# Performance work log

Hardware: AMD Instinct MI355X
Metric: run time of the kernel (lower is better)

## Reference

```python
import jax, jax.numpy as jnp
import numpy as np

NEG_SLOPE = 0.2
EPS = 1e-16


def gat_conv(x, edge_index, W, att_src, att_dst, bias, heads, out_ch, concat):
    """PyG-style GATConv (eval mode, add_self_loops=True)."""
    N = x.shape[0]
    h = (x @ W).reshape(N, heads, out_ch)              # [N,H,C]
    loop = jnp.arange(N, dtype=edge_index.dtype)
    src = jnp.concatenate([edge_index[0], loop])       # [E+N]
    dst = jnp.concatenate([edge_index[1], loop])
    a_src = jnp.sum(h * att_src, axis=-1)              # [N,H]
    a_dst = jnp.sum(h * att_dst, axis=-1)
    e = jax.nn.leaky_relu(a_src[src] + a_dst[dst], NEG_SLOPE)  # [E+N,H]
    # segment softmax over destination nodes
    m = jax.ops.segment_max(e, dst, num_segments=N)
    e = jnp.exp(e - m[dst])
    s = jax.ops.segment_sum(e, dst, num_segments=N)
    alpha = e / (s[dst] + EPS)                         # [E+N,H]
    msg = h[src] * alpha[..., None]                    # [E+N,H,C]
    out = jax.ops.segment_sum(msg, dst, num_segments=N)  # [N,H,C]
    out = out.reshape(N, heads * out_ch) if concat else out.mean(axis=1)
    return out + bias


def setup_inputs() -> dict:
    key = jax.random.key(0)
    ks = jax.random.split(key, 11)
    N, F, E = 100000, 128, 1600000
    H1, C1 = 4, 16
    H2, C2 = 1, 16
    return {
        "x": jax.random.normal(ks[0], (N, F), dtype=jnp.float32),
        "edge_index": jax.random.randint(ks[1], (2, E), 0, N, dtype=jnp.int64) if jax.config.jax_enable_x64 else jax.random.randint(ks[1], (2, E), 0, N).astype(jnp.int32),
        "W1": jax.random.normal(ks[2], (F, H1 * C1), dtype=jnp.float32) * 0.1,
        "att_src1": jax.random.normal(ks[3], (H1, C1), dtype=jnp.float32) * 0.1,
        "att_dst1": jax.random.normal(ks[4], (H1, C1), dtype=jnp.float32) * 0.1,
        "bias1": jax.random.normal(ks[5], (H1 * C1,), dtype=jnp.float32) * 0.1,
        "W2": jax.random.normal(ks[6], (H1 * C1, H2 * C2), dtype=jnp.float32) * 0.1,
        "att_src2": jax.random.normal(ks[7], (H2, C2), dtype=jnp.float32) * 0.1,
        "att_dst2": jax.random.normal(ks[8], (H2, C2), dtype=jnp.float32) * 0.1,
        "bias2": jax.random.normal(ks[9], (C2,), dtype=jnp.float32) * 0.1,
    }


def reference(x, edge_index, W1, att_src1, att_dst1, bias1, W2, att_src2, att_dst2, bias2):
    # dropout is identity in eval mode
    h = gat_conv(x, edge_index, W1, att_src1, att_dst1, bias1, heads=4, out_ch=16, concat=True)
    h = jax.nn.elu(h)
    h = gat_conv(h, edge_index, W2, att_src2, att_dst2, bias2, heads=1, out_ch=16, concat=False)
    return jax.nn.log_softmax(h, axis=1)
```

## Files before the change

kernel.cpp:

```cpp
#include <hip/hip_runtime.h>
#include <hip/hip_fp16.h>
#include <hip/hip_bf16.h>
#include <math.h>


#define LRELU(v) ((v) > 0.f ? (v) : 0.2f * (v))
#define BSH 8
#define BCAP 5120
#define CHK 8192

typedef __attribute__((ext_vector_type(8))) short short8;
typedef __attribute__((ext_vector_type(8))) _Float16 half8;
typedef __attribute__((ext_vector_type(4))) _Float16 half4;
typedef __attribute__((ext_vector_type(4))) float float4v;

static __device__ __forceinline__ short f2bf(float f) {
    __hip_bfloat16 b = __float2bfloat16(f);
    return *reinterpret_cast<short*>(&b);
}

__global__ __launch_bounds__(256) void k_pre(const int* __restrict__ ei, int* __restrict__ cursor,
                                             int* __restrict__ stage, int E, int NBK,
                                             const float* __restrict__ x,
                                             const float* __restrict__ W1,
                                             const float* __restrict__ att_src1,
                                             const float* __restrict__ att_dst1,
                                             __half* __restrict__ h1,
                                             float* __restrict__ a_src, float* __restrict__ a_dst,
                                             int N, int GS) {
    __shared__ __align__(16) char smem[80 * 136 * 2];
    int tid = threadIdx.x;
    if (blockIdx.x < GS) {
        int* hist = (int*)smem;
        int* cnt2 = hist + 512;
        int* base = cnt2 + 512;
        int e0 = blockIdx.x * CHK;
        int nedge = E - e0; if (nedge > CHK) nedge = CHK;
        for (int i = tid; i < 512; i += 256) { hist[i] = 0; cnt2[i] = 0; }
        __syncthreads();
        for (int j = tid; j < nedge; j += 256) {
            int d = ei[E + e0 + j];
            atomicAdd(&hist[d >> BSH], 1);
        }
        __syncthreads();
        for (int b = tid; b < NBK; b += 256) {
            int c = hist[b];
            if (c > 0) base[b] = b * BCAP + atomicAdd(&cursor[b], c);
        }
        __syncthreads();
        for (int j = tid; j < nedge; j += 256) {
            int s = ei[e0 + j];
            int d = ei[E + e0 + j];
            int b = d >> BSH;
            int r = atomicAdd(&cnt2[b], 1);
            stage[base[b] + r] = s | ((d & ((1 << BSH) - 1)) << 17);
        }
    } else {
        short* wt = (short*)smem;
        for (int i = tid; i < 128 * 64; i += 256) {
            int k = i >> 6, c = i & 63;
            wt[c * 136 + k] = f2bf(W1[i]);
        }
        for (int i = tid; i < 16 * 128; i += 256) {
            int col = i >> 7, k = i & 127;
            float v = 0.f;
            if (col < 8) {
                int h = col & 3;
                const float* att = (col < 4) ? att_src1 : att_dst1;
                #pragma unroll
                for (int c = 0; c < 16; c++) v += W1[k * 64 + h * 16 + c] * att[h * 16 + c];
            }
            wt[(64 + col) * 136 + k] = f2bf(v);
        }
        __syncthreads();
        int wave = tid >> 6, lane = tid & 63;
        int m = lane & 15, q = lane >> 4;
        int nbase = (blockIdx.x - GS) * 64 + wave * 16;
        int anode = nbase + m;
        bool rowok = anode < N;
        const float* xrow = x + (size_t)(rowok ? anode : 0) * 128 + q * 8;

        float4v acc[5];
        #pragma unroll
        for (int ct = 0; ct < 5; ct++)
            #pragma unroll
            for (int r = 0; r < 4; r++) acc[ct][r] = 0.f;

        #pragma unroll
        for (int kc = 0; kc < 4; kc++) {
            float4 u0 = make_float4(0.f, 0.f, 0.f, 0.f), u1 = u0;
            if (rowok) {
                u0 = *(const float4*)(xrow + kc * 32);
                u1 = *(const float4*)(xrow + kc * 32 + 4);
            }
            short8 af;
            af[0] = f2bf(u0.x); af[1] = f2bf(u0.y); af[2] = f2bf(u0.z); af[3] = f2bf(u0.w);
            af[4] = f2bf(u1.x); af[5] = f2bf(u1.y); af[6] = f2bf(u1.z); af[7] = f2bf(u1.w);
            #pragma unroll
            for (int ct = 0; ct < 5; ct++) {
                short8 bf = *(const short8*)&wt[(ct * 16 + m) * 136 + kc * 32 + q * 8];
                acc[ct] = __builtin_amdgcn_mfma_f32_16x16x32_bf16(af, bf, acc[ct], 0, 0, 0);
            }
        }
        #pragma unroll
        for (int ct = 0; ct < 4; ct++) {
            #pragma unroll
            for (int r = 0; r < 4; r++) {
                int n = nbase + q * 4 + r;
                if (n < N) h1[(size_t)n * 64 + ct * 16 + m] = __float2half(acc[ct][r]);
            }
        }
        #pragma unroll
        for (int r = 0; r < 4; r++) {
            int n = nbase + q * 4 + r;
            if (n < N) {
                float v = acc[4][r];
                if (m < 4) a_src[n * 4 + m] = v;
                else if (m < 8) a_dst[n * 4 + (m - 4)] = v;
            }
        }
    }
}

__global__ __launch_bounds__(256) void k_build(const int* __restrict__ stage,
                                               const int* __restrict__ cursor,
                                               int* __restrict__ row_start,
                                               int* __restrict__ csr,
                                               int NBK, int E, int N) {
    __shared__ int cnt[256];
    __shared__ int lb[256];
    __shared__ int cur[256];
    __shared__ int sA[256];
    int b = blockIdx.x, tid = threadIdx.x;
    int nodes0 = b << BSH;
    int nnodes = N - nodes0; if (nnodes > 256) nnodes = 256;
    int partial = 0;
    for (int i = tid; i < b; i += 256) partial += cursor[i];
    sA[tid] = partial;
    __syncthreads();
    for (int off = 128; off >= 1; off >>= 1) {
        if (tid < off) sA[tid] += sA[tid + off];
        __syncthreads();
    }
    int ebase = sA[0];
    int ecnt = cursor[b];
    __syncthreads();
    if (b == 0 && tid == 0) row_start[N] = E + N;
    const int* sbk = stage + b * BCAP;
    cnt[tid] = (tid < nnodes) ? 1 : 0;
    __syncthreads();
    for (int e = tid; e < ecnt; e += 256) {
        int l = (sbk[e] >> 17) & 255;
        atomicAdd(&cnt[l], 1);
    }
    __syncthreads();
    int myc = cnt[tid];
    sA[tid] = myc;
    __syncthreads();
    for (int off = 1; off < 256; off <<= 1) {
        int r = sA[tid] + ((tid >= off) ? sA[tid - off] : 0);
        __syncthreads();
        sA[tid] = r;
        __syncthreads();
    }
    int gb = ebase + nodes0;
    lb[tid] = sA[tid] - myc;
    cur[tid] = 1;
    __syncthreads();
    if (tid < nnodes) {
        row_start[nodes0 + tid] = gb + lb[tid];
        csr[gb + lb[tid]] = nodes0 + tid;
    }
    __syncthreads();
    for (int e = tid; e < ecnt; e += 256) {
        int v = sbk[e];
        int l = (v >> 17) & 255;
        int src = v & 0x1FFFF;
        int r = atomicAdd(&cur[l], 1);
        csr[gb + lb[l] + r] = src;
    }
}

__global__ __launch_bounds__(256) void k_agg1f(const int* __restrict__ row_start,
                                               const int* __restrict__ csr_src,
                                               const float* __restrict__ a_src,
                                               const float* __restrict__ a_dst,
                                               const __half* __restrict__ h1,
                                               const float* __restrict__ bias,
                                               const float* __restrict__ W2,
                                               const float* __restrict__ att_src2,
                                               const float* __restrict__ att_dst2,
                                               __half* __restrict__ h2,
                                               float* __restrict__ a_src2,
                                               float* __restrict__ a_dst2, int N) {
    __shared__ float sW2[64 * 16];
    __shared__ float sAs[16], sAd[16];
    int tid = threadIdx.x;
    for (int i = tid; i < 1024; i += 256) sW2[i] = W2[i];
    if (tid < 16) { sAs[tid] = att_src2[tid]; sAd[tid] = att_dst2[tid]; }
    __syncthreads();
    int wave = tid >> 6, lane = tid & 63;
    int grp = lane >> 3, sub = lane & 3, par = (lane >> 2) & 1;
    int node = blockIdx.x * 32 + wave * 8 + grp;
    if (node >= N) return;
    int row = row_start[node];
    int deg = row_start[node + 1] - row;
    float adm = a_dst[node * 4 + sub];
    const _Float16* hb = (const _Float16*)h1 + sub * 16;
    const int* cp = csr_src + row + par;
    float A[16];
    #pragma unroll
    for (int c = 0; c < 16; c++) A[c] = 0.f;
    float sh = 0.f;
    int c0 = 0, c1 = 0, c2 = 0, c3 = 0;
    if (deg >= 8) { c0 = cp[0]; c1 = cp[2]; c2 = cp[4]; c3 = cp[6]; }
    int j = 0;
    for (; j + 8 <= deg; j += 8) {
        int s0 = c0, s1 = c1, s2 = c2, s3 = c3;
        float x0 = a_src[s0 * 4 + sub] + adm;
        float x1 = a_src[s1 * 4 + sub] + adm;
        float x2 = a_src[s2 * 4 + sub] + adm;
        float x3 = a_src[s3 * 4 + sub] + adm;
        half8 p0 = *(const half8*)(hb + (size_t)s0 * 64);
        half8 q0 = *(const half8*)(hb + (size_t)s0 * 64 + 8);
        half8 p1 = *(const half8*)(hb + (size_t)s1 * 64);
        half8 q1 = *(const half8*)(hb + (size_t)s1 * 64 + 8);
        half8 p2 = *(const half8*)(hb + (size_t)s2 * 64);
        half8 q2 = *(const half8*)(hb + (size_t)s2 * 64 + 8);
        half8 p3 = *(const half8*)(hb + (size_t)s3 * 64);
        half8 q3 = *(const half8*)(hb + (size_t)s3 * 64 + 8);
        if (j + 16 <= deg) {
            c0 = cp[j + 8]; c1 = cp[j + 10]; c2 = cp[j + 12]; c3 = cp[j + 14];
        }
        float e0 = __expf(fmaxf(x0, 0.2f * x0));
        float e1 = __expf(fmaxf(x1, 0.2f * x1));
        float e2 = __expf(fmaxf(x2, 0.2f * x2));
        float e3 = __expf(fmaxf(x3, 0.2f * x3));
        sh += (e0 + e1) + (e2 + e3);
        #pragma unroll
        for (int c = 0; c < 8; c++) {
            A[c]     += e0 * (float)p0[c] + e1 * (float)p1[c]
                      + e2 * (float)p2[c] + e3 * (float)p3[c];
            A[c + 8] += e0 * (float)q0[c] + e1 * (float)q1[c]
                      + e2 * (float)q2[c] + e3 * (float)q3[c];
        }
    }
    for (; j < deg; j += 2) {
        int idx = j + par;
        if (idx < deg) {
            int s = csr_src[row + idx];
            float xv = a_src[s * 4 + sub] + adm;
            half8 p = *(const half8*)(hb + (size_t)s * 64);
            half8 q = *(const half8*)(hb + (size_t)s * 64 + 8);
            float e = __expf(fmaxf(xv, 0.2f * xv));
            sh += e;
            #pragma unroll
            for (int c = 0; c < 8; c++) {
                A[c]     += e * (float)p[c];
                A[c + 8] += e * (float)q[c];
            }
        }
    }
    sh += __shfl_xor(sh, 4, 64);
    #pragma unroll
    for (int c = 0; c < 16; c++) A[c] += __shfl_xor(A[c], 4, 64);
    float iv = 1.f / (sh + 1e-16f);
    const float4* bb = (const float4*)bias + sub * 4;
    float o[16];
    #pragma unroll
    for (int c4 = 0; c4 < 4; c4++) {
        float4 b = bb[c4];
        float o0 = A[c4 * 4 + 0] * iv + b.x;
        float o1 = A[c4 * 4 + 1] * iv + b.y;
        float o2 = A[c4 * 4 + 2] * iv + b.z;
        float o3 = A[c4 * 4 + 3] * iv + b.w;
        o[c4 * 4 + 0] = (o0 > 0.f) ? o0 : (__expf(o0) - 1.f);
        o[c4 * 4 + 1] = (o1 > 0.f) ? o1 : (__expf(o1) - 1.f);
        o[c4 * 4 + 2] = (o2 > 0.f) ? o2 : (__expf(o2) - 1.f);
        o[c4 * 4 + 3] = (o3 > 0.f) ? o3 : (__expf(o3) - 1.f);
    }
    float pk[8];
    #pragma unroll
    for (int kk = 0; kk < 8; kk++) pk[kk] = 0.f;
    #pragma unroll
    for (int cc = 0; cc < 16; cc++) {
        float ov = o[cc];
        const float* wr = &sW2[(sub * 16 + cc) * 16 + par * 8];
        #pragma unroll
        for (int kk = 0; kk < 8; kk++) pk[kk] += ov * wr[kk];
    }
    #pragma unroll
    for (int kk = 0; kk < 8; kk++) {
        pk[kk] += __shfl_xor(pk[kk], 1, 64);
        pk[kk] += __shfl_xor(pk[kk], 2, 64);
    }
    if (sub == 0) {
        union { __half2 hh[4]; float4 f; } u;
        u.hh[0] = __floats2half2_rn(pk[0], pk[1]);
        u.hh[1] = __floats2half2_rn(pk[2], pk[3]);
        u.hh[2] = __floats2half2_rn(pk[4], pk[5]);
        u.hh[3] = __floats2half2_rn(pk[6], pk[7]);
        *(float4*)&h2[(size_t)node * 16 + par * 8] = u.f;
    }
    float ps = 0.f, pd = 0.f;
    #pragma unroll
    for (int kk = 0; kk < 8; kk++) {
        ps += pk[kk] * sAs[par * 8 + kk];
        pd += pk[kk] * sAd[par * 8 + kk];
    }
    ps += __shfl_xor(ps, 4, 64);
    pd += __shfl_xor(pd, 4, 64);
    if (sub == 0 && par == 0) { a_src2[node] = ps; a_dst2[node] = pd; }
}

__global__ __launch_bounds__(256) void k_agg2(const int* __restrict__ row_start,
                                              const int* __restrict__ csr_src,
                                              const float* __restrict__ a_src,
                                              const float* __restrict__ a_dst,
                                              const __half* __restrict__ h2,
                                              const float* __restrict__ bias,
                                              float* __restrict__ out, int N) {
    int tid = threadIdx.x;
    int wave = tid >> 6, lane = tid & 63;
    int grp = lane >> 4, sub = lane & 3, par = (lane >> 2) & 3;
    int node = blockIdx.x * 16 + wave * 4 + grp;
    if (node >= N) return;
    int row = row_start[node];
    int deg = row_start[node + 1] - row;
    float ad = a_dst[node];
    const _Float16* hb = (const _Float16*)h2 + sub * 4;
    const int* cp = csr_src + row + par;
    float A0 = 0.f, A1 = 0.f, A2 = 0.f, A3 = 0.f;
    float sh = 0.f;
    int c0 = 0, c1 = 0, c2 = 0, c3 = 0;
    if (deg >= 16) { c0 = cp[0]; c1 = cp[4]; c2 = cp[8]; c3 = cp[12]; }
    int j = 0;
    for (; j + 16 <= deg; j += 16) {
        int s0 = c0, s1 = c1, s2 = c2, s3 = c3;
        float x0 = a_src[s0] + ad;
        float x1 = a_src[s1] + ad;
        float x2 = a_src[s2] + ad;
        float x3 = a_src[s3] + ad;
        half4 v0 = *(const half4*)(hb + (size_t)s0 * 16);
        half4 v1 = *(const half4*)(hb + (size_t)s1 * 16);
        half4 v2 = *(const half4*)(hb + (size_t)s2 * 16);
        half4 v3 = *(const half4*)(hb + (size_t)s3 * 16);
        if (j + 32 <= deg) {
            c0 = cp[j + 16]; c1 = cp[j + 20]; c2 = cp[j + 24]; c3 = cp[j + 28];
        }
        float e0 = __expf(fmaxf(x0, 0.2f * x0));
        float e1 = __expf(fmaxf(x1, 0.2f * x1));
        float e2 = __expf(fmaxf(x2, 0.2f * x2));
        float e3 = __expf(fmaxf(x3, 0.2f * x3));
        sh += (e0 + e1) + (e2 + e3);
        A0 += e0 * (float)v0[0] + e1 * (float)v1[0] + e2 * (float)v2[0] + e3 * (float)v3[0];
        A1 += e0 * (float)v0[1] + e1 * (float)v1[1] + e2 * (float)v2[1] + e3 * (float)v3[1];
        A2 += e0 * (float)v0[2] + e1 * (float)v1[2] + e2 * (float)v2[2] + e3 * (float)v3[2];
        A3 += e0 * (float)v0[3] + e1 * (float)v1[3] + e2 * (float)v2[3] + e3 * (float)v3[3];
    }
    for (; j < deg; j += 4) {
        int idx = j + par;
        if (idx < deg) {
            int s = csr_src[row + idx];
            float xv = a_src[s] + ad;
            half4 v = *(const half4*)(hb + (size_t)s * 16);
            float e = __expf(fmaxf(xv, 0.2f * xv));
            sh += e;
            A0 += e * (float)v[0];
            A1 += e * (float)v[1];
            A2 += e * (float)v[2];
            A3 += e * (float)v[3];
        }
    }
    sh += __shfl_xor(sh, 4, 64);  sh += __shfl_xor(sh, 8, 64);
    A0 += __shfl_xor(A0, 4, 64);  A0 += __shfl_xor(A0, 8, 64);
    A1 += __shfl_xor(A1, 4, 64);  A1 += __shfl_xor(A1, 8, 64);
    A2 += __shfl_xor(A2, 4, 64);  A2 += __shfl_xor(A2, 8, 64);
    A3 += __shfl_xor(A3, 4, 64);  A3 += __shfl_xor(A3, 8, 64);
    float iv = 1.f / (sh + 1e-16f);
    float4 b = ((const float4*)bias)[sub];
    float v0 = A0 * iv + b.x;
    float v1 = A1 * iv + b.y;
    float v2 = A2 * iv + b.z;
    float v3 = A3 * iv + b.w;
    float mx = fmaxf(fmaxf(v0, v1), fmaxf(v2, v3));
    mx = fmaxf(mx, __shfl_xor(mx, 1, 64));
    mx = fmaxf(mx, __shfl_xor(mx, 2, 64));
    float se = __expf(v0 - mx) + __expf(v1 - mx) + __expf(v2 - mx) + __expf(v3 - mx);
    se += __shfl_xor(se, 1, 64);
    se += __shfl_xor(se, 2, 64);
    float ls = mx + __logf(se);
    if (par == 0)
        *(float4*)&out[(size_t)node * 16 + sub * 4] =
            make_float4(v0 - ls, v1 - ls, v2 - ls, v3 - ls);
}

extern "C" void kernel_launch(void* const* d_in, const int* in_sizes, int n_in,
                              void* d_out, int out_size, void* d_ws, size_t ws_size,
                              hipStream_t stream) {
    const float* x        = (const float*)d_in[0];
    const int*   ei       = (const int*)d_in[1];
    const float* W1       = (const float*)d_in[2];
    const float* att_src1 = (const float*)d_in[3];
    const float* att_dst1 = (const float*)d_in[4];
    const float* bias1    = (const float*)d_in[5];
    const float* W2       = (const float*)d_in[6];
    const float* att_src2 = (const float*)d_in[7];
    const float* att_dst2 = (const float*)d_in[8];
    const float* bias2    = (const float*)d_in[9];
    float* out = (float*)d_out;

    const int N = in_sizes[0] / 128;
    const int E = in_sizes[1] / 2;
    const int NBK = (N + 255) >> BSH;
    const int GS = (E + CHK - 1) / CHK;
    const int GG = (N + 63) / 64;

    char* p = (char*)d_ws;
    auto alloc = [&](size_t bytes) -> void* {
        void* r = (void*)p;
        p += (bytes + 255) & ~(size_t)255;
        return r;
    };
    __half* h1     = (__half*)alloc((size_t)N * 64 * 2);
    __half* h2     = (__half*)alloc((size_t)N * 16 * 2);
    float* a_src1  = (float*)alloc((size_t)N * 4 * 4);
    float* a_dst1  = (float*)alloc((size_t)N * 4 * 4);
    float* a_src2  = (float*)alloc((size_t)N * 4);
    float* a_dst2  = (float*)alloc((size_t)N * 4);
    int*   row_st  = (int*)alloc((size_t)(N + 1) * 4);
    int*   csr     = (int*)alloc((size_t)(E + N) * 4);
    int*   stage   = (int*)alloc((size_t)NBK * BCAP * 4);
    int*   cursor  = (int*)alloc((size_t)NBK * 4);
    (void)ws_size; (void)n_in; (void)out_size;

    hipMemsetAsync(cursor, 0, (size_t)NBK * 4, stream);
    k_pre<<<GS + GG, 256, 0, stream>>>(ei, cursor, stage, E, NBK,
                                       x, W1, att_src1, att_dst1,
                                       h1, a_src1, a_dst1, N, GS);
    k_build<<<NBK, 256, 0, stream>>>(stage, cursor, row_st, csr, NBK, E, N);
    k_agg1f<<<(N + 31) / 32, 256, 0, stream>>>(row_st, csr, a_src1, a_dst1, h1, bias1,
                                               W2, att_src2, att_dst2,
                                               h2, a_src2, a_dst2, N);
    k_agg2<<<(N + 15) / 16, 256, 0, stream>>>(row_st, csr, a_src2, a_dst2, h2, bias2, out, N);
}
```

Before: 229.9 us.

## Replace bucketed staging CSR build with global-atomic count, scan and fill

The CSR construction changes from a two-level scheme (block-local histograms into 256-node buckets in a staging buffer, then a per-bucket local sort) to a plain counting sort. Per-node global atomics count in-degrees, two scan kernels compute row starts and place self-loops, and a fill kernel scatters sources with global atomicAdd on per-node cursors. This drops the staging buffer and its extra read/write pass, but puts 1.6M global atomics into each of two passes, adds kernel launches, and makes neighbor order within a row nondeterministic.

```diff
diff --git a/kernel.cpp b/kernel.cpp
--- a/kernel.cpp
+++ b/kernel.cpp
@@ -5,9 +5,6 @@
 
 
 #define LRELU(v) ((v) > 0.f ? (v) : 0.2f * (v))
-#define BSH 8
-#define BCAP 5120
-#define CHK 8192
 
 typedef __attribute__((ext_vector_type(8))) short short8;
 typedef __attribute__((ext_vector_type(8))) _Float16 half8;
@@ -19,44 +16,32 @@
     return *reinterpret_cast<short*>(&b);
 }
 
-__global__ __launch_bounds__(256) void k_pre(const int* __restrict__ ei, int* __restrict__ cursor,
-                                             int* __restrict__ stage, int E, int NBK,
+__global__ __launch_bounds__(256) void k_pre(const int* __restrict__ ei, int* __restrict__ cnt,
+                                             int E,
                                              const float* __restrict__ x,
                                              const float* __restrict__ W1,
                                              const float* __restrict__ att_src1,
                                              const float* __restrict__ att_dst1,
                                              __half* __restrict__ h1,
                                              float* __restrict__ a_src, float* __restrict__ a_dst,
-                                             int N, int GS) {
-    __shared__ __align__(16) char smem[80 * 136 * 2];
+                                             int N, int DG) {
+    __shared__ __align__(16) short wt[80 * 136];
     int tid = threadIdx.x;
-    if (blockIdx.x < GS) {
-        int* hist = (int*)smem;
-        int* cnt2 = hist + 512;
-        int* base = cnt2 + 512;
-        int e0 = blockIdx.x * CHK;
-        int nedge = E - e0; if (nedge > CHK) nedge = CHK;
-        for (int i = tid; i < 512; i += 256) { hist[i] = 0; cnt2[i] = 0; }
-        __syncthreads();
-        for (int j = tid; j < nedge; j += 256) {
-            int d = ei[E + e0 + j];
-            atomicAdd(&hist[d >> BSH], 1);
-        }
-        __syncthreads();
-        for (int b = tid; b < NBK; b += 256) {
-            int c = hist[b];
-            if (c > 0) base[b] = b * BCAP + atomicAdd(&cursor[b], c);
-        }
-        __syncthreads();
-        for (int j = tid; j < nedge; j += 256) {
-            int s = ei[e0 + j];
-            int d = ei[E + e0 + j];
-            int b = d >> BSH;
-            int r = atomicAdd(&cnt2[b], 1);
-            stage[base[b] + r] = s | ((d & ((1 << BSH) - 1)) << 17);
-        }
+    if (blockIdx.x < DG) {
+        const int* dst = ei + E;
+        int gid = blockIdx.x * 256 + tid;
+        int gsz = DG * 256;
+        int EV4 = E >> 2;
+        for (int i = gid; i < EV4; i += gsz) {
+            int4 d = ((const int4*)dst)[i];
+            atomicAdd(&cnt[d.x], 1);
+            atomicAdd(&cnt[d.y], 1);
+            atomicAdd(&cnt[d.z], 1);
+            atomicAdd(&cnt[d.w], 1);
+        }
+        int rem = E & 3;
+        if (gid < rem) atomicAdd(&cnt[dst[EV4 * 4 + gid]], 1);
     } else {
-        short* wt = (short*)smem;
         for (int i = tid; i < 128 * 64; i += 256) {
             int k = i >> 6, c = i & 63;
             wt[c * 136 + k] = f2bf(W1[i]);
@@ -75,7 +60,7 @@
         __syncthreads();
         int wave = tid >> 6, lane = tid & 63;
         int m = lane & 15, q = lane >> 4;
-        int nbase = (blockIdx.x - GS) * 64 + wave * 16;
+        int nbase = (blockIdx.x - DG) * 64 + wave * 16;
         int anode = nbase + m;
         bool rowok = anode < N;
         const float* xrow = x + (size_t)(rowok ? anode : 0) * 128 + q * 8;
@@ -122,62 +107,77 @@
     }
 }
 
-__global__ __launch_bounds__(256) void k_build(const int* __restrict__ stage,
-                                               const int* __restrict__ cursor,
-                                               int* __restrict__ row_start,
-                                               int* __restrict__ csr,
-                                               int NBK, int E, int N) {
-    __shared__ int cnt[256];
-    __shared__ int lb[256];
-    __shared__ int cur[256];
+__global__ __launch_bounds__(256) void k_scan1(const int* __restrict__ cnt,
+                                               int* __restrict__ partial, int N) {
     __shared__ int sA[256];
-    int b = blockIdx.x, tid = threadIdx.x;
-    int nodes0 = b << BSH;
-    int nnodes = N - nodes0; if (nnodes > 256) nnodes = 256;
-    int partial = 0;
-    for (int i = tid; i < b; i += 256) partial += cursor[i];
-    sA[tid] = partial;
+    int tid = threadIdx.x;
+    int n = blockIdx.x * 256 + tid;
+    sA[tid] = (n < N) ? cnt[n] + 1 : 0;
     __syncthreads();
     for (int off = 128; off >= 1; off >>= 1) {
         if (tid < off) sA[tid] += sA[tid + off];
         __syncthreads();
     }
-    int ebase = sA[0];
-    int ecnt = cursor[b];
+    if (tid == 0) partial[blockIdx.x] = sA[0];
+}
+
+__global__ __launch_bounds__(256) void k_scan2(int* __restrict__ cnt,
+                                               const int* __restrict__ partial,
+                                               int* __restrict__ row_start,
+                                               int* __restrict__ csr, int N) {
+    __shared__ int sA[256];
+    int tid = threadIdx.x;
+    int b = blockIdx.x;
+    int ps = 0;
+    for (int i = tid; i < b; i += 256) ps += partial[i];
+    sA[tid] = ps;
     __syncthreads();
-    if (b == 0 && tid == 0) row_start[N] = E + N;
-    const int* sbk = stage + b * BCAP;
-    cnt[tid] = (tid < nnodes) ? 1 : 0;
+    for (int off = 128; off >= 1; off >>= 1) {
+        if (tid < off) sA[tid] += sA[tid + off];
+        __syncthreads();
+    }
+    int base = sA[0];
     __syncthreads();
-    for (int e = tid; e < ecnt; e += 256) {
-        int l = (sbk[e] >> 17) & 255;
-        atomicAdd(&cnt[l], 1);
-    }
-    __syncthreads();
-    int myc = cnt[tid];
-    sA[tid] = myc;
+    int n = b * 256 + tid;
+    int w = (n < N) ? cnt[n] + 1 : 0;
+    sA[tid] = w;
     __syncthreads();
     for (int off = 1; off < 256; off <<= 1) {
-        int r = sA[tid] + ((tid >= off) ? sA[tid - off] : 0);
+        int v = sA[tid] + ((tid >= off) ? sA[tid - off] : 0);
         __syncthreads();
-        sA[tid] = r;
+        sA[tid] = v;
         __syncthreads();
     }
-    int gb = ebase + nodes0;
-    lb[tid] = sA[tid] - myc;
-    cur[tid] = 1;
-    __syncthreads();
-    if (tid < nnodes) {
-        row_start[nodes0 + tid] = gb + lb[tid];
-        csr[gb + lb[tid]] = nodes0 + tid;
-    }
-    __syncthreads();
-    for (int e = tid; e < ecnt; e += 256) {
-        int v = sbk[e];
-        int l = (v >> 17) & 255;
-        int src = v & 0x1FFFF;
-        int r = atomicAdd(&cur[l], 1);
-        csr[gb + lb[l] + r] = src;
+    int rs = base + sA[tid] - w;
+    if (n < N) {
+        row_start[n] = rs;
+        csr[rs] = n;
+        cnt[n] = rs + 1;
+        if (n == N - 1) row_start[N] = rs + w;
+    }
+}
+
+__global__ __launch_bounds__(256) void k_fill(const int* __restrict__ ei,
+                                              int* __restrict__ cnt,
+                                              int* __restrict__ csr, int E) {
+    const int* src = ei;
+    const int* dst = ei + E;
+    int gid = blockIdx.x * 256 + threadIdx.x;
+    int gsz = gridDim.x * 256;
+    int EV4 = E >> 2;
+    for (int i = gid; i < EV4; i += gsz) {
+        int4 s = ((const int4*)src)[i];
+        int4 d = ((const int4*)dst)[i];
+        int p0 = atomicAdd(&cnt[d.x], 1); csr[p0] = s.x;
+        int p1 = atomicAdd(&cnt[d.y], 1); csr[p1] = s.y;
+        int p2 = atomicAdd(&cnt[d.z], 1); csr[p2] = s.z;
+        int p3 = atomicAdd(&cnt[d.w], 1); csr[p3] = s.w;
+    }
+    int rem = E & 3;
+    if (gid < rem) {
+        int e = EV4 * 4 + gid;
+        int p = atomicAdd(&cnt[dst[e]], 1);
+        csr[p] = src[e];
     }
 }
 
@@ -412,9 +412,10 @@
 
     const int N = in_sizes[0] / 128;
     const int E = in_sizes[1] / 2;
-    const int NBK = (N + 255) >> BSH;
-    const int GS = (E + CHK - 1) / CHK;
+    const int NS = (N + 255) / 256;
+    const int DG = 512;
     const int GG = (N + 63) / 64;
+    const int FG = 1024;
 
     char* p = (char*)d_ws;
     auto alloc = [&](size_t bytes) -> void* {
@@ -430,15 +431,16 @@
     float* a_dst2  = (float*)alloc((size_t)N * 4);
     int*   row_st  = (int*)alloc((size_t)(N + 1) * 4);
     int*   csr     = (int*)alloc((size_t)(E + N) * 4);
-    int*   stage   = (int*)alloc((size_t)NBK * BCAP * 4);
-    int*   cursor  = (int*)alloc((size_t)NBK * 4);
+    int*   cnt     = (int*)alloc((size_t)N * 4);
+    int*   partial = (int*)alloc((size_t)NS * 4);
     (void)ws_size; (void)n_in; (void)out_size;
 
-    hipMemsetAsync(cursor, 0, (size_t)NBK * 4, stream);
-    k_pre<<<GS + GG, 256, 0, stream>>>(ei, cursor, stage, E, NBK,
-                                       x, W1, att_src1, att_dst1,
-                                       h1, a_src1, a_dst1, N, GS);
-    k_build<<<NBK, 256, 0, stream>>>(stage, cursor, row_st, csr, NBK, E, N);
+    hipMemsetAsync(cnt, 0, (size_t)N * 4, stream);
+    k_pre<<<DG + GG, 256, 0, stream>>>(ei, cnt, E, x, W1, att_src1, att_dst1,
+                                       h1, a_src1, a_dst1, N, DG);
+    k_scan1<<<NS, 256, 0, stream>>>(cnt, partial, N);
+    k_scan2<<<NS, 256, 0, stream>>>(cnt, partial, row_st, csr, N);
+    k_fill<<<FG, 256, 0, stream>>>(ei, cnt, csr, E);
     k_agg1f<<<(N + 31) / 32, 256, 0, stream>>>(row_st, csr, a_src1, a_dst1, h1, bias1,
                                                W2, att_src2, att_dst2,
                                                h2, a_src2, a_dst2, N);
```

Measured after the change: 370.8 us. 1.61x slower.

## Widen per-node lane groups in layer-1 aggregation and vectorize CSR build loads

Applied to the files above, without the earlier changes.

The layer-1 aggregation kernel now gives each destination node 16 lanes instead of 8, so four edge partitions run in parallel per node. The partials are merged with an extra shuffle stage, and the W2 projection is split into 4-column slices per partition. Separately, the CSR build kernel reads staged edges as int4 vectors and handles the tail scalarly, which cuts load instructions. More lanes per node improves latency hiding for gathers at average degree around 17, but adds reduction shuffles and idle lanes on low-degree nodes.

```diff
diff --git a/kernel.cpp b/kernel.cpp
--- a/kernel.cpp
+++ b/kernel.cpp
@@ -149,10 +149,15 @@
     const int* sbk = stage + b * BCAP;
     cnt[tid] = (tid < nnodes) ? 1 : 0;
     __syncthreads();
-    for (int e = tid; e < ecnt; e += 256) {
-        int l = (sbk[e] >> 17) & 255;
-        atomicAdd(&cnt[l], 1);
-    }
+    int e4 = ecnt & ~3;
+    for (int e = tid * 4; e < e4; e += 1024) {
+        int4 v = *(const int4*)&sbk[e];
+        atomicAdd(&cnt[(v.x >> 17) & 255], 1);
+        atomicAdd(&cnt[(v.y >> 17) & 255], 1);
+        atomicAdd(&cnt[(v.z >> 17) & 255], 1);
+        atomicAdd(&cnt[(v.w >> 17) & 255], 1);
+    }
+    if (tid < (ecnt & 3)) atomicAdd(&cnt[(sbk[e4 + tid] >> 17) & 255], 1);
     __syncthreads();
     int myc = cnt[tid];
     sA[tid] = myc;
@@ -172,12 +177,19 @@
         csr[gb + lb[tid]] = nodes0 + tid;
     }
     __syncthreads();
-    for (int e = tid; e < ecnt; e += 256) {
-        int v = sbk[e];
+    for (int e = tid * 4; e < e4; e += 1024) {
+        int4 v = *(const int4*)&sbk[e];
+        int l, r;
+        l = (v.x >> 17) & 255; r = atomicAdd(&cur[l], 1); csr[gb + lb[l] + r] = v.x & 0x1FFFF;
+        l = (v.y >> 17) & 255; r = atomicAdd(&cur[l], 1); csr[gb + lb[l] + r] = v.y & 0x1FFFF;
+        l = (v.z >> 17) & 255; r = atomicAdd(&cur[l], 1); csr[gb + lb[l] + r] = v.z & 0x1FFFF;
+        l = (v.w >> 17) & 255; r = atomicAdd(&cur[l], 1); csr[gb + lb[l] + r] = v.w & 0x1FFFF;
+    }
+    if (tid < (ecnt & 3)) {
+        int v = sbk[e4 + tid];
         int l = (v >> 17) & 255;
-        int src = v & 0x1FFFF;
         int r = atomicAdd(&cur[l], 1);
-        csr[gb + lb[l] + r] = src;
+        csr[gb + lb[l] + r] = v & 0x1FFFF;
     }
 }
 
@@ -200,8 +212,8 @@
     if (tid < 16) { sAs[tid] = att_src2[tid]; sAd[tid] = att_dst2[tid]; }
     __syncthreads();
     int wave = tid >> 6, lane = tid & 63;
-    int grp = lane >> 3, sub = lane & 3, par = (lane >> 2) & 1;
-    int node = blockIdx.x * 32 + wave * 8 + grp;
+    int grp = lane >> 4, sub = lane & 3, par = (lane >> 2) & 3;
+    int node = blockIdx.x * 16 + wave * 4 + grp;
     if (node >= N) return;
     int row = row_start[node];
     int deg = row_start[node + 1] - row;
@@ -213,9 +225,9 @@
     for (int c = 0; c < 16; c++) A[c] = 0.f;
     float sh = 0.f;
     int c0 = 0, c1 = 0, c2 = 0, c3 = 0;
-    if (deg >= 8) { c0 = cp[0]; c1 = cp[2]; c2 = cp[4]; c3 = cp[6]; }
+    if (deg >= 16) { c0 = cp[0]; c1 = cp[4]; c2 = cp[8]; c3 = cp[12]; }
     int j = 0;
-    for (; j + 8 <= deg; j += 8) {
+    for (; j + 16 <= deg; j += 16) {
         int s0 = c0, s1 = c1, s2 = c2, s3 = c3;
         float x0 = a_src[s0 * 4 + sub] + adm;
         float x1 = a_src[s1 * 4 + sub] + adm;
@@ -229,8 +241,8 @@
         half8 q2 = *(const half8*)(hb + (size_t)s2 * 64 + 8);
         half8 p3 = *(const half8*)(hb + (size_t)s3 * 64);
         half8 q3 = *(const half8*)(hb + (size_t)s3 * 64 + 8);
-        if (j + 16 <= deg) {
-            c0 = cp[j + 8]; c1 = cp[j + 10]; c2 = cp[j + 12]; c3 = cp[j + 14];
+        if (j + 32 <= deg) {
+            c0 = cp[j + 16]; c1 = cp[j + 20]; c2 = cp[j + 24]; c3 = cp[j + 28];
         }
         float e0 = __expf(fmaxf(x0, 0.2f * x0));
         float e1 = __expf(fmaxf(x1, 0.2f * x1));
@@ -245,7 +257,7 @@
                       + e2 * (float)q2[c] + e3 * (float)q3[c];
         }
     }
-    for (; j < deg; j += 2) {
+    for (; j < deg; j += 4) {
         int idx = j + par;
         if (idx < deg) {
             int s = csr_src[row + idx];
@@ -261,9 +273,12 @@
             }
         }
     }
-    sh += __shfl_xor(sh, 4, 64);
-    #pragma unroll
-    for (int c = 0; c < 16; c++) A[c] += __shfl_xor(A[c], 4, 64);
+    sh += __shfl_xor(sh, 4, 64);  sh += __shfl_xor(sh, 8, 64);
+    #pragma unroll
+    for (int c = 0; c < 16; c++) {
+        A[c] += __shfl_xor(A[c], 4, 64);
+        A[c] += __shfl_xor(A[c], 8, 64);
+    }
     float iv = 1.f / (sh + 1e-16f);
     const float4* bb = (const float4*)bias + sub * 4;
     float o[16];
@@ -279,37 +294,33 @@
         o[c4 * 4 + 2] = (o2 > 0.f) ? o2 : (__expf(o2) - 1.f);
         o[c4 * 4 + 3] = (o3 > 0.f) ? o3 : (__expf(o3) - 1.f);
     }
-    float pk[8];
-    #pragma unroll
-    for (int kk = 0; kk < 8; kk++) pk[kk] = 0.f;
+    float pk[4] = {0.f, 0.f, 0.f, 0.f};
     #pragma unroll
     for (int cc = 0; cc < 16; cc++) {
         float ov = o[cc];
-        const float* wr = &sW2[(sub * 16 + cc) * 16 + par * 8];
-        #pragma unroll
-        for (int kk = 0; kk < 8; kk++) pk[kk] += ov * wr[kk];
-    }
-    #pragma unroll
-    for (int kk = 0; kk < 8; kk++) {
+        const float* wr = &sW2[(sub * 16 + cc) * 16 + par * 4];
+        #pragma unroll
+        for (int kk = 0; kk < 4; kk++) pk[kk] += ov * wr[kk];
+    }
+    #pragma unroll
+    for (int kk = 0; kk < 4; kk++) {
         pk[kk] += __shfl_xor(pk[kk], 1, 64);
         pk[kk] += __shfl_xor(pk[kk], 2, 64);
     }
     if (sub == 0) {
-        union { __half2 hh[4]; float4 f; } u;
+        union { __half2 hh[2]; float2 f; } u;
         u.hh[0] = __floats2half2_rn(pk[0], pk[1]);
         u.hh[1] = __floats2half2_rn(pk[2], pk[3]);
-        u.hh[2] = __floats2half2_rn(pk[4], pk[5]);
-        u.hh[3] = __floats2half2_rn(pk[6], pk[7]);
-        *(float4*)&h2[(size_t)node * 16 + par * 8] = u.f;
+        *(float2*)&h2[(size_t)node * 16 + par * 4] = u.f;
     }
     float ps = 0.f, pd = 0.f;
     #pragma unroll
-    for (int kk = 0; kk < 8; kk++) {
-        ps += pk[kk] * sAs[par * 8 + kk];
-        pd += pk[kk] * sAd[par * 8 + kk];
-    }
-    ps += __shfl_xor(ps, 4, 64);
-    pd += __shfl_xor(pd, 4, 64);
+    for (int kk = 0; kk < 4; kk++) {
+        ps += pk[kk] * sAs[par * 4 + kk];
+        pd += pk[kk] * sAd[par * 4 + kk];
+    }
+    ps += __shfl_xor(ps, 4, 64);  ps += __shfl_xor(ps, 8, 64);
+    pd += __shfl_xor(pd, 4, 64);  pd += __shfl_xor(pd, 8, 64);
     if (sub == 0 && par == 0) { a_src2[node] = ps; a_dst2[node] = pd; }
 }
 
@@ -439,7 +450,7 @@
                                        x, W1, att_src1, att_dst1,
                                        h1, a_src1, a_dst1, N, GS);
     k_build<<<NBK, 256, 0, stream>>>(stage, cursor, row_st, csr, NBK, E, N);
-    k_agg1f<<<(N + 31) / 32, 256, 0, stream>>>(row_st, csr, a_src1, a_dst1, h1, bias1,
+    k_agg1f<<<(N + 15) / 16, 256, 0, stream>>>(row_st, csr, a_src1, a_dst1, h1, bias1,
                                                W2, att_src2, att_dst2,
                                                h2, a_src2, a_dst2, N);
     k_agg2<<<(N + 15) / 16, 256, 0, stream>>>(row_st, csr, a_src2, a_dst2, h2, bias2, out, N);
```

Result: slower. 234.6 us (+2.0%).
